# Kernel tuning notes

Measured on AMD Instinct MI355X. Metric: run time of the kernel, lower is better.

The kernel has to match this reference:

```python
import jax, jax.numpy as jnp
import numpy as np

B, N1, N2, E = 8, 32, 32, 256
H = 8                 # num_heads == args.vir_heads
KD = E // H           # key dim per head = 32
HD = E // H           # head dim (value_dim == embed_dim)
L = N1 * N2           # 1024 tokens
SCALING = KD ** -0.5
LN_EPS = 1e-5


def _rel_pos_2d():
    # RetNetRelPosDeform2D with zero offsets (vir_use_deformable=False)
    half = 1.0 / 10000.0 ** jnp.linspace(0.0, 1.0, KD // 2)
    angle = jnp.repeat(half, 2)                                   # (KD,) interleaved pairs
    decay = jnp.log(1.0 - 2.0 ** (-2.0 - 5.0 * jnp.arange(H, dtype=jnp.float32) / H))  # (H,)
    i1 = jnp.arange(N1, dtype=jnp.float32)
    i2 = jnp.arange(N2, dtype=jnp.float32)
    index_k = (i1[:, None] + i2[None, :]).reshape(L)              # (L,)
    sin_k = jnp.sin(index_k[:, None] * angle[None, :])            # (L, KD)
    cos_k = jnp.cos(index_k[:, None] * angle[None, :])
    # zero offsets => index_q == index_k, broadcast over (B, H)
    sin_q = sin_k[None, None]                                     # (1,1,L,KD)
    cos_q = cos_k[None, None]
    # Manhattan distance decay mask on the 2D grid
    d = (jnp.abs(i1[:, None, None, None] - i1[None, None, :, None])
         + jnp.abs(i2[None, :, None, None] - i2[None, None, None, :])).reshape(L, L)
    mask = jnp.exp(d[None, :, :] * decay[:, None, None])          # (H, L, L)
    mask = jnp.nan_to_num(mask)
    mask = mask / jnp.sqrt(mask.sum(-1, keepdims=True))
    return sin_q, cos_q, sin_k, cos_k, mask


def rotate_every_two(x):
    x1 = x[..., ::2]
    x2 = x[..., 1::2]
    return jnp.stack((-x2, x1), axis=-1).reshape(x.shape)


def theta_shift(x, sin, cos):
    return x * cos + rotate_every_two(x) * sin


def setup_inputs() -> dict:
    key = jax.random.key(0)
    ks = jax.random.split(key, 5)
    gain_qkv = 2.0 ** -2.5 * (6.0 / (E + E)) ** 0.5  # xavier_uniform bound scale
    gain_o = 2.0 ** -1 * (6.0 / (E + E)) ** 0.5
    x = jax.random.normal(ks[0], (B, N1, N2, E), dtype=jnp.float32)
    Wq = jax.random.uniform(ks[1], (E, E), jnp.float32, -gain_qkv, gain_qkv)
    Wk = jax.random.uniform(ks[2], (E, E), jnp.float32, -gain_qkv, gain_qkv)
    Wv = jax.random.uniform(ks[3], (E, E), jnp.float32, -gain_qkv, gain_qkv)
    Wo = jax.random.uniform(ks[4], (E, E), jnp.float32, -gain_o, gain_o)
    ln_g = jnp.ones((HD,), jnp.float32)
    ln_b = jnp.zeros((HD,), jnp.float32)
    return {"x": x, "Wq": Wq, "Wk": Wk, "Wv": Wv, "Wo": Wo, "ln_g": ln_g, "ln_b": ln_b}


def reference(x, Wq, Wk, Wv, Wo, ln_g, ln_b):
    sin_q, cos_q, sin_k, cos_k, mask = _rel_pos_2d()
    xf = x.reshape(B, L, E)
    q = (xf @ Wq.T).reshape(B, L, H, KD).transpose(0, 2, 1, 3)    # (B,H,L,KD)
    k = (xf @ Wk.T * SCALING).reshape(B, L, H, KD).transpose(0, 2, 1, 3)
    vr = (xf @ Wv.T).reshape(B, L, H, HD).transpose(0, 2, 1, 3)   # (B,H,L,HD)
    qr = theta_shift(q, sin_q, cos_q)
    kr = theta_shift(k, sin_k[None, None], cos_k[None, None])
    qk = jnp.einsum('bhqd,bhkd->bhqk', qr, kr) * mask[None]       # (B,H,L,L)
    den = jnp.clip(jax.lax.stop_gradient(jnp.abs(qk)).sum(-1, keepdims=True), 1.0, 5e4)
    qk = qk / den
    out = jnp.einsum('bhqk,bhkd->bhqd', qk, vr).transpose(0, 2, 1, 3)  # (B,L,H,HD)
    mu = out.mean(-1, keepdims=True)
    var = out.var(-1, keepdims=True)
    out = (out - mu) / jnp.sqrt(var + LN_EPS) * ln_g + ln_b       # per-head LayerNorm
    out = jax.nn.gelu(out.reshape(B, L, H * HD), approximate=False)
    out = out @ Wo.T
    return out.reshape(B, N1, N2, E)
```

## Files before the change

kernel.cpp:

```cpp
#include <hip/hip_runtime.h>
#include <math.h>

typedef unsigned short u16;
typedef unsigned int u32;
typedef __bf16 bf16x8 __attribute__((ext_vector_type(8)));
typedef float f32x4 __attribute__((ext_vector_type(4)));

#define SCALING 0.17677669529663687f
#define LOG2E 1.44269504088896f
#define LOG2_10000 13.287712379549449f

__device__ __forceinline__ u16 f2bf(float f) {
    u32 u; __builtin_memcpy(&u, &f, 4);
    u = u + 0x7FFFu + ((u >> 16) & 1u);
    return (u16)(u >> 16);
}
__device__ __forceinline__ u32 fbits(float f) {
    u32 u; __builtin_memcpy(&u, &f, 4); return u;
}
__device__ __forceinline__ u32 pack_bf16(float lo, float hi) {
    return __builtin_amdgcn_perm(fbits(hi) + 0x8000u, fbits(lo) + 0x8000u, 0x07060302u);
}
__device__ __forceinline__ f32x4 mfma16(bf16x8 a, bf16x8 b, f32x4 c) {
    return __builtin_amdgcn_mfma_f32_16x16x32_bf16(a, b, c, 0, 0, 0);
}
__device__ __forceinline__ float decay_l2(int h) {
    return logf(1.0f - exp2f(-2.0f - 0.625f * (float)h)) * LOG2E;
}

__global__ __launch_bounds__(256) void cvt_kernel(
    const float* __restrict__ x,
    const float* __restrict__ Wq, const float* __restrict__ Wk,
    const float* __restrict__ Wv, const float* __restrict__ Wo,
    u16* __restrict__ xb, u16* __restrict__ wb) {
    int bid = blockIdx.x;
    const float* src; u16* dst; int off;
    if (bid < 1024) { src = x; dst = xb; off = bid * 2048; }
    else {
        int wsel = (bid - 1024) >> 5;
        src = (wsel == 0) ? Wq : (wsel == 1) ? Wk : (wsel == 2) ? Wv : Wo;
        dst = wb + wsel * 65536;
        off = ((bid - 1024) & 31) * 2048;
    }
    int i = off + threadIdx.x * 8;
    float4 a = *(const float4*)&src[i];
    float4 b = *(const float4*)&src[i + 4];
    union { int4 v; u16 s[8]; } t;
    t.s[0] = f2bf(a.x); t.s[1] = f2bf(a.y); t.s[2] = f2bf(a.z); t.s[3] = f2bf(a.w);
    t.s[4] = f2bf(b.x); t.s[5] = f2bf(b.y); t.s[6] = f2bf(b.z); t.s[7] = f2bf(b.w);
    *(int4*)&dst[i] = t.v;
}

__global__ __launch_bounds__(256) void gemm_bt_kernel(
    const u16* __restrict__ A, const u16* __restrict__ Wb,
    u16* __restrict__ O0, u16* __restrict__ O1, u16* __restrict__ O2,
    float* __restrict__ Of, int mode_base) {
    __shared__ __align__(16) u16 As[64 * 136];
    __shared__ __align__(16) u16 Ws[64 * 136];
    int z = blockIdx.z;
    const u16* W = Wb + z * 65536;
    u16* O = (z == 0) ? O0 : (z == 1) ? O1 : O2;
    int mode = mode_base + z;
    int n0 = blockIdx.x * 64, r0 = blockIdx.y * 64;
    int tid = threadIdx.x;
    int w = tid >> 6, lane = tid & 63, ln = lane & 15, quad = lane >> 4;
    f32x4 acc[4] = {};
#pragma unroll
    for (int ch = 0; ch < 2; ch++) {
        int k0 = ch * 128;
        if (ch) __syncthreads();
#pragma unroll
        for (int i = 0; i < 4; i++) {
            int c = tid + i * 256;
            int row = c >> 4, seg = c & 15;
            *(int4*)&As[row * 136 + seg * 8] = *(const int4*)&A[(long)(r0 + row) * 256 + k0 + seg * 8];
            *(int4*)&Ws[row * 136 + seg * 8] = *(const int4*)&W[(long)(n0 + row) * 256 + k0 + seg * 8];
        }
        __syncthreads();
#pragma unroll
        for (int kt = 0; kt < 4; kt++) {
            bf16x8 a = *(const bf16x8*)&As[(w * 16 + ln) * 136 + kt * 32 + quad * 8];
#pragma unroll
            for (int nt = 0; nt < 4; nt++) {
                bf16x8 b = *(const bf16x8*)&Ws[(nt * 16 + ln) * 136 + kt * 32 + quad * 8];
                acc[nt] = mfma16(a, b, acc[nt]);
            }
        }
    }
    int rowg = r0 + w * 16 + quad * 4;
    if (mode == 3) {
#pragma unroll
        for (int nt = 0; nt < 4; nt++) {
            int e = n0 + nt * 16 + ln;
#pragma unroll
            for (int r = 0; r < 4; r++)
                Of[(long)(rowg + r) * 256 + e] = acc[nt][r];
        }
        return;
    }
    float scl = (mode == 1) ? SCALING : 1.0f;
#pragma unroll
    for (int nt = 0; nt < 4; nt++) {
        int e = n0 + nt * 16 + ln;
        int d = e & 31, hh = e >> 5;
        float ang = exp2f(-LOG2_10000 * (1.0f / 15.0f) * (float)(d >> 1));
#pragma unroll
        for (int r = 0; r < 4; r++) {
            int gi = rowg + r;
            int b = gi >> 10, l = gi & 1023;
            float v = acc[nt][r] * scl;
            float p = __shfl_xor(v, 1);
            float res;
            if (mode == 2) {
                res = v;
            } else {
                float idx = (float)((l >> 5) + (l & 31));
                float sv, cv;
                __sincosf(idx * ang, &sv, &cv);
                res = (d & 1) ? (v * cv + p * sv) : (v * cv - p * sv);
            }
            O[(((long)(b * 8 + hh)) * 1024 + l) * 32 + d] = f2bf(res);
        }
    }
}

__global__ __launch_bounds__(256) void attn_kernel(
    const u16* __restrict__ qr, const u16* __restrict__ kr, const u16* __restrict__ vr,
    const float* __restrict__ lng, const float* __restrict__ lnb,
    u16* __restrict__ out) {
    __shared__ __align__(16) u16 Qs[64 * 40];
    __shared__ __align__(16) u16 Ks[2][64 * 40];
    __shared__ __align__(16) u32 VtW[2][32 * 36];
    __shared__ __align__(16) u32 PsW[4][16 * 36];
    __shared__ float Tt[64];
    __shared__ float Ss[32];
    __shared__ float lngS[32], lnbS[32];
    int b = blockIdx.z, h = blockIdx.y, q0 = blockIdx.x * 64;
    int tid = threadIdx.x, w = tid >> 6, lane = tid & 63, ln = lane & 15, quad = lane >> 4;
    long bh = b * 8 + h;
    const u16* qb = qr + bh * 32768;
    const u16* kb = kr + bh * 32768;
    const u16* vb = vr + bh * 32768;
    float dec = decay_l2(h);
    {
        int row = tid >> 2, seg = tid & 3;
        *(int4*)&Qs[row * 40 + seg * 8] = *(const int4*)&qb[(q0 + row) * 32 + seg * 8];
    }
    if (tid < 63) Tt[tid] = exp2f(dec * (float)tid);
    if (tid >= 64 && tid < 96) { lngS[tid - 64] = lng[tid - 64]; lnbS[tid - 64] = lnb[tid - 64]; }
    int krow = tid >> 2, kseg = tid & 3;
    int vp = tid >> 3, vseg = tid & 7;
    int4 kreg = *(const int4*)&kb[(long)krow * 32 + kseg * 8];
    int2 v0 = *(const int2*)&vb[(long)(vp * 2) * 32 + vseg * 4];
    int2 v1 = *(const int2*)&vb[(long)(vp * 2 + 1) * 32 + vseg * 4];
    __syncthreads();
    if (tid < 32) {
        float s = 0.0f;
#pragma unroll
        for (int b2 = 0; b2 < 32; b2++) s += Tt[abs(tid - b2)];
        Ss[tid] = s;
    }
    *(int4*)&Ks[0][krow * 40 + kseg * 8] = kreg;
    VtW[0][(vseg * 4 + 0) * 36 + vp] = __builtin_amdgcn_perm(v1.x, v0.x, 0x05040100u);
    VtW[0][(vseg * 4 + 1) * 36 + vp] = __builtin_amdgcn_perm(v1.x, v0.x, 0x07060302u);
    VtW[0][(vseg * 4 + 2) * 36 + vp] = __builtin_amdgcn_perm(v1.y, v0.y, 0x05040100u);
    VtW[0][(vseg * 4 + 3) * 36 + vp] = __builtin_amdgcn_perm(v1.y, v0.y, 0x07060302u);
    kreg = *(const int4*)&kb[(long)(64 + krow) * 32 + kseg * 8];
    v0 = *(const int2*)&vb[(long)(64 + vp * 2) * 32 + vseg * 4];
    v1 = *(const int2*)&vb[(long)(64 + vp * 2 + 1) * 32 + vseg * 4];
    __syncthreads();
    int q = q0 + w * 16 + ln;
    int q1i = q >> 5, q2i = q & 31;
    float rqv = rsqrtf(Ss[q1i] * Ss[q2i]);
    bf16x8 aq = *(const bf16x8*)&Qs[(w * 16 + ln) * 40 + quad * 8];
    float bt[2][4];
#pragma unroll
    for (int s2 = 0; s2 < 2; s2++)
#pragma unroll
        for (int r = 0; r < 4; r++)
            bt[s2][r] = Tt[abs(q2i - (s2 * 16 + quad * 4 + r))];
    f32x4 accO0 = {}, accO1 = {};
    float den = 0.0f;
    u32* psw = &PsW[w][0];
    for (int kt = 0; kt < 16; kt++) {
        int cur = kt & 1;
        float a0 = Tt[abs(q1i - 2 * kt)] * rqv;
        float a1 = Tt[abs(q1i - 2 * kt - 1)] * rqv;
        const u16* ksb = &Ks[cur][0];
        const u32* vtb = &VtW[cur][0];
#pragma unroll
        for (int nt = 0; nt < 4; nt++) {
            bf16x8 ak = *(const bf16x8*)&ksb[(nt * 16 + ln) * 40 + quad * 8];
            f32x4 s = mfma16(ak, aq, (f32x4){0.f, 0.f, 0.f, 0.f});
            float aa = (nt & 2) ? a1 : a0;
            float p0 = s[0] * aa * bt[nt & 1][0];
            float p1 = s[1] * aa * bt[nt & 1][1];
            float p2 = s[2] * aa * bt[nt & 1][2];
            float p3 = s[3] * aa * bt[nt & 1][3];
            den += fabsf(p0); den += fabsf(p1); den += fabsf(p2); den += fabsf(p3);
            int2 pw;
            pw.x = (int)pack_bf16(p0, p1);
            pw.y = (int)pack_bf16(p2, p3);
            *(int2*)&psw[ln * 36 + nt * 8 + quad * 2] = pw;
        }
#pragma unroll
        for (int c = 0; c < 2; c++) {
            bf16x8 bp  = *(const bf16x8*)&psw[ln * 36 + c * 16 + quad * 4];
            bf16x8 av0 = *(const bf16x8*)&vtb[(ln)      * 36 + c * 16 + quad * 4];
            bf16x8 av1 = *(const bf16x8*)&vtb[(16 + ln) * 36 + c * 16 + quad * 4];
            accO0 = mfma16(av0, bp, accO0);
            accO1 = mfma16(av1, bp, accO1);
        }
        if (kt < 15) {
            int nb = 1 - cur;
            *(int4*)&Ks[nb][krow * 40 + kseg * 8] = kreg;
            VtW[nb][(vseg * 4 + 0) * 36 + vp] = __builtin_amdgcn_perm(v1.x, v0.x, 0x05040100u);
            VtW[nb][(vseg * 4 + 1) * 36 + vp] = __builtin_amdgcn_perm(v1.x, v0.x, 0x07060302u);
            VtW[nb][(vseg * 4 + 2) * 36 + vp] = __builtin_amdgcn_perm(v1.y, v0.y, 0x05040100u);
            VtW[nb][(vseg * 4 + 3) * 36 + vp] = __builtin_amdgcn_perm(v1.y, v0.y, 0x07060302u);
            if (kt < 14) {
                int t2 = (kt + 2) * 64;
                kreg = *(const int4*)&kb[(long)(t2 + krow) * 32 + kseg * 8];
                v0 = *(const int2*)&vb[(long)(t2 + vp * 2) * 32 + vseg * 4];
                v1 = *(const int2*)&vb[(long)(t2 + vp * 2 + 1) * 32 + vseg * 4];
            }
            __syncthreads();
        }
    }
    den += __shfl_xor(den, 16);
    den += __shfl_xor(den, 32);
    float id = 1.0f / fminf(fmaxf(den, 1.0f), 50000.0f);
    float o[8];
#pragma unroll
    for (int r = 0; r < 4; r++) { o[r] = accO0[r] * id; o[4 + r] = accO1[r] * id; }
    float s1 = 0.0f, s2 = 0.0f;
#pragma unroll
    for (int i = 0; i < 8; i++) { s1 += o[i]; s2 += o[i] * o[i]; }
    s1 += __shfl_xor(s1, 16); s1 += __shfl_xor(s1, 32);
    s2 += __shfl_xor(s2, 16); s2 += __shfl_xor(s2, 32);
    float mean = s1 * (1.0f / 32.0f);
    float var = s2 * (1.0f / 32.0f) - mean * mean;
    float rstd = rsqrtf(var + 1e-5f);
    float xg[8];
#pragma unroll
    for (int nv = 0; nv < 2; nv++)
#pragma unroll
        for (int r = 0; r < 4; r++) {
            int d = nv * 16 + quad * 4 + r;
            float xv = (o[nv * 4 + r] - mean) * rstd * lngS[d] + lnbS[d];
            xg[nv * 4 + r] = 0.5f * xv * (1.0f + erff(xv * 0.70710678118654752f));
        }
    u16* orow = out + ((long)(b * 1024 + q)) * 256 + h * 32;
    int2 st0, st1;
    st0.x = (int)pack_bf16(xg[0], xg[1]); st0.y = (int)pack_bf16(xg[2], xg[3]);
    st1.x = (int)pack_bf16(xg[4], xg[5]); st1.y = (int)pack_bf16(xg[6], xg[7]);
    *(int2*)&orow[quad * 4] = st0;
    *(int2*)&orow[16 + quad * 4] = st1;
}

extern "C" void kernel_launch(void* const* d_in, const int* in_sizes, int n_in,
                              void* d_out, int out_size, void* d_ws, size_t ws_size,
                              hipStream_t stream) {
    const float* x   = (const float*)d_in[0];
    const float* Wq  = (const float*)d_in[1];
    const float* Wk  = (const float*)d_in[2];
    const float* Wv  = (const float*)d_in[3];
    const float* Wo  = (const float*)d_in[4];
    const float* lng = (const float*)d_in[5];
    const float* lnb = (const float*)d_in[6];
    float* outp = (float*)d_out;

    u16* xb   = (u16*)d_ws;
    u16* wb   = xb + 2097152;
    u16* qr   = wb + 262144;
    u16* kr   = qr + 2097152;
    u16* vr   = kr + 2097152;
    u16* attn = vr + 2097152;

    cvt_kernel<<<1152, 256, 0, stream>>>(x, Wq, Wk, Wv, Wo, xb, wb);
    gemm_bt_kernel<<<dim3(4, 128, 3), 256, 0, stream>>>(xb, wb, qr, kr, vr, nullptr, 0);
    attn_kernel<<<dim3(16, 8, 8), 256, 0, stream>>>(qr, kr, vr, lng, lnb, attn);
    gemm_bt_kernel<<<dim3(4, 128, 1), 256, 0, stream>>>(attn, wb + 3 * 65536, nullptr, nullptr, nullptr, outp, 3);
}
```

Baseline: 114.8 us.

## Split attention key tiles across two wave groups and precompute rotary table

After: 134.2 us. +16.9%, slower.

```diff
diff --git a/kernel.cpp b/kernel.cpp
--- a/kernel.cpp
+++ b/kernel.cpp
@@ -32,8 +32,18 @@
     const float* __restrict__ x,
     const float* __restrict__ Wq, const float* __restrict__ Wk,
     const float* __restrict__ Wv, const float* __restrict__ Wo,
-    u16* __restrict__ xb, u16* __restrict__ wb) {
+    u16* __restrict__ xb, u16* __restrict__ wb, float2* __restrict__ tc) {
     int bid = blockIdx.x;
+    if (bid >= 1152) {
+        int idx = (bid - 1152) * 256 + threadIdx.x;
+        int l = idx >> 5, d = idx & 31;
+        float ang = exp2f(-LOG2_10000 * (1.0f / 15.0f) * (float)(d >> 1));
+        float idl = (float)((l >> 5) + (l & 31));
+        float sv, cv;
+        __sincosf(idl * ang, &sv, &cv);
+        tc[idx] = make_float2(cv, (d & 1) ? sv : -sv);
+        return;
+    }
     const float* src; u16* dst; int off;
     if (bid < 1024) { src = x; dst = xb; off = bid * 2048; }
     else {
@@ -53,6 +63,7 @@
 
 __global__ __launch_bounds__(256) void gemm_bt_kernel(
     const u16* __restrict__ A, const u16* __restrict__ Wb,
+    const float2* __restrict__ tc,
     u16* __restrict__ O0, u16* __restrict__ O1, u16* __restrict__ O2,
     float* __restrict__ Of, int mode_base) {
     __shared__ __align__(16) u16 As[64 * 136];
@@ -103,7 +114,6 @@
     for (int nt = 0; nt < 4; nt++) {
         int e = n0 + nt * 16 + ln;
         int d = e & 31, hh = e >> 5;
-        float ang = exp2f(-LOG2_10000 * (1.0f / 15.0f) * (float)(d >> 1));
 #pragma unroll
         for (int r = 0; r < 4; r++) {
             int gi = rowg + r;
@@ -114,45 +124,49 @@
             if (mode == 2) {
                 res = v;
             } else {
-                float idx = (float)((l >> 5) + (l & 31));
-                float sv, cv;
-                __sincosf(idx * ang, &sv, &cv);
-                res = (d & 1) ? (v * cv + p * sv) : (v * cv - p * sv);
+                float2 sc = tc[l * 32 + d];
+                res = v * sc.x + p * sc.y;
             }
             O[(((long)(b * 8 + hh)) * 1024 + l) * 32 + d] = f2bf(res);
         }
     }
 }
 
-__global__ __launch_bounds__(256) void attn_kernel(
+__global__ __launch_bounds__(512) void attn_kernel(
     const u16* __restrict__ qr, const u16* __restrict__ kr, const u16* __restrict__ vr,
     const float* __restrict__ lng, const float* __restrict__ lnb,
     u16* __restrict__ out) {
     __shared__ __align__(16) u16 Qs[64 * 40];
     __shared__ __align__(16) u16 Ks[2][64 * 40];
     __shared__ __align__(16) u32 VtW[2][32 * 36];
-    __shared__ __align__(16) u32 PsW[4][16 * 36];
+    __shared__ __align__(16) u32 PsW[8][16 * 20];
     __shared__ float Tt[64];
     __shared__ float Ss[32];
     __shared__ float lngS[32], lnbS[32];
     int b = blockIdx.z, h = blockIdx.y, q0 = blockIdx.x * 64;
     int tid = threadIdx.x, w = tid >> 6, lane = tid & 63, ln = lane & 15, quad = lane >> 4;
+    int wa = w & 3;
+    int half = w >> 2;
     long bh = b * 8 + h;
     const u16* qb = qr + bh * 32768;
     const u16* kb = kr + bh * 32768;
     const u16* vb = vr + bh * 32768;
     float dec = decay_l2(h);
-    {
+    if (tid < 256) {
         int row = tid >> 2, seg = tid & 3;
         *(int4*)&Qs[row * 40 + seg * 8] = *(const int4*)&qb[(q0 + row) * 32 + seg * 8];
     }
     if (tid < 63) Tt[tid] = exp2f(dec * (float)tid);
     if (tid >= 64 && tid < 96) { lngS[tid - 64] = lng[tid - 64]; lnbS[tid - 64] = lnb[tid - 64]; }
     int krow = tid >> 2, kseg = tid & 3;
-    int vp = tid >> 3, vseg = tid & 7;
-    int4 kreg = *(const int4*)&kb[(long)krow * 32 + kseg * 8];
-    int2 v0 = *(const int2*)&vb[(long)(vp * 2) * 32 + vseg * 4];
-    int2 v1 = *(const int2*)&vb[(long)(vp * 2 + 1) * 32 + vseg * 4];
+    int vt = tid - 256, vp = vt >> 3, vseg = vt & 7;
+    int4 kreg; int2 v0, v1;
+    if (tid < 256) {
+        kreg = *(const int4*)&kb[(long)krow * 32 + kseg * 8];
+    } else {
+        v0 = *(const int2*)&vb[(long)(vp * 2) * 32 + vseg * 4];
+        v1 = *(const int2*)&vb[(long)(vp * 2 + 1) * 32 + vseg * 4];
+    }
     __syncthreads();
     if (tid < 32) {
         float s = 0.0f;
@@ -160,19 +174,22 @@
         for (int b2 = 0; b2 < 32; b2++) s += Tt[abs(tid - b2)];
         Ss[tid] = s;
     }
-    *(int4*)&Ks[0][krow * 40 + kseg * 8] = kreg;
-    VtW[0][(vseg * 4 + 0) * 36 + vp] = __builtin_amdgcn_perm(v1.x, v0.x, 0x05040100u);
-    VtW[0][(vseg * 4 + 1) * 36 + vp] = __builtin_amdgcn_perm(v1.x, v0.x, 0x07060302u);
-    VtW[0][(vseg * 4 + 2) * 36 + vp] = __builtin_amdgcn_perm(v1.y, v0.y, 0x05040100u);
-    VtW[0][(vseg * 4 + 3) * 36 + vp] = __builtin_amdgcn_perm(v1.y, v0.y, 0x07060302u);
-    kreg = *(const int4*)&kb[(long)(64 + krow) * 32 + kseg * 8];
-    v0 = *(const int2*)&vb[(long)(64 + vp * 2) * 32 + vseg * 4];
-    v1 = *(const int2*)&vb[(long)(64 + vp * 2 + 1) * 32 + vseg * 4];
+    if (tid < 256) {
+        *(int4*)&Ks[0][krow * 40 + kseg * 8] = kreg;
+        kreg = *(const int4*)&kb[(long)(64 + krow) * 32 + kseg * 8];
+    } else {
+        VtW[0][(vseg * 4 + 0) * 36 + vp] = __builtin_amdgcn_perm(v1.x, v0.x, 0x05040100u);
+        VtW[0][(vseg * 4 + 1) * 36 + vp] = __builtin_amdgcn_perm(v1.x, v0.x, 0x07060302u);
+        VtW[0][(vseg * 4 + 2) * 36 + vp] = __builtin_amdgcn_perm(v1.y, v0.y, 0x05040100u);
+        VtW[0][(vseg * 4 + 3) * 36 + vp] = __builtin_amdgcn_perm(v1.y, v0.y, 0x07060302u);
+        v0 = *(const int2*)&vb[(long)(64 + vp * 2) * 32 + vseg * 4];
+        v1 = *(const int2*)&vb[(long)(64 + vp * 2 + 1) * 32 + vseg * 4];
+    }
     __syncthreads();
-    int q = q0 + w * 16 + ln;
+    int q = q0 + wa * 16 + ln;
     int q1i = q >> 5, q2i = q & 31;
     float rqv = rsqrtf(Ss[q1i] * Ss[q2i]);
-    bf16x8 aq = *(const bf16x8*)&Qs[(w * 16 + ln) * 40 + quad * 8];
+    bf16x8 aq = *(const bf16x8*)&Qs[(wa * 16 + ln) * 40 + quad * 8];
     float bt[2][4];
 #pragma unroll
     for (int s2 = 0; s2 < 2; s2++)
@@ -184,78 +201,95 @@
     u32* psw = &PsW[w][0];
     for (int kt = 0; kt < 16; kt++) {
         int cur = kt & 1;
-        float a0 = Tt[abs(q1i - 2 * kt)] * rqv;
-        float a1 = Tt[abs(q1i - 2 * kt - 1)] * rqv;
+        float aa = Tt[abs(q1i - 2 * kt - half)] * rqv;
         const u16* ksb = &Ks[cur][0];
         const u32* vtb = &VtW[cur][0];
 #pragma unroll
-        for (int nt = 0; nt < 4; nt++) {
+        for (int j = 0; j < 2; j++) {
+            int nt = 2 * half + j;
             bf16x8 ak = *(const bf16x8*)&ksb[(nt * 16 + ln) * 40 + quad * 8];
             f32x4 s = mfma16(ak, aq, (f32x4){0.f, 0.f, 0.f, 0.f});
-            float aa = (nt & 2) ? a1 : a0;
-            float p0 = s[0] * aa * bt[nt & 1][0];
-            float p1 = s[1] * aa * bt[nt & 1][1];
-            float p2 = s[2] * aa * bt[nt & 1][2];
-            float p3 = s[3] * aa * bt[nt & 1][3];
+            float p0 = s[0] * aa * bt[j][0];
+            float p1 = s[1] * aa * bt[j][1];
+            float p2 = s[2] * aa * bt[j][2];
+            float p3 = s[3] * aa * bt[j][3];
             den += fabsf(p0); den += fabsf(p1); den += fabsf(p2); den += fabsf(p3);
             int2 pw;
             pw.x = (int)pack_bf16(p0, p1);
             pw.y = (int)pack_bf16(p2, p3);
-            *(int2*)&psw[ln * 36 + nt * 8 + quad * 2] = pw;
-        }
-#pragma unroll
-        for (int c = 0; c < 2; c++) {
-            bf16x8 bp  = *(const bf16x8*)&psw[ln * 36 + c * 16 + quad * 4];
-            bf16x8 av0 = *(const bf16x8*)&vtb[(ln)      * 36 + c * 16 + quad * 4];
-            bf16x8 av1 = *(const bf16x8*)&vtb[(16 + ln) * 36 + c * 16 + quad * 4];
+            *(int2*)&psw[ln * 20 + j * 8 + quad * 2] = pw;
+        }
+        {
+            bf16x8 bp  = *(const bf16x8*)&psw[ln * 20 + quad * 4];
+            bf16x8 av0 = *(const bf16x8*)&vtb[(ln)      * 36 + half * 16 + quad * 4];
+            bf16x8 av1 = *(const bf16x8*)&vtb[(16 + ln) * 36 + half * 16 + quad * 4];
             accO0 = mfma16(av0, bp, accO0);
             accO1 = mfma16(av1, bp, accO1);
         }
         if (kt < 15) {
             int nb = 1 - cur;
-            *(int4*)&Ks[nb][krow * 40 + kseg * 8] = kreg;
-            VtW[nb][(vseg * 4 + 0) * 36 + vp] = __builtin_amdgcn_perm(v1.x, v0.x, 0x05040100u);
-            VtW[nb][(vseg * 4 + 1) * 36 + vp] = __builtin_amdgcn_perm(v1.x, v0.x, 0x07060302u);
-            VtW[nb][(vseg * 4 + 2) * 36 + vp] = __builtin_amdgcn_perm(v1.y, v0.y, 0x05040100u);
-            VtW[nb][(vseg * 4 + 3) * 36 + vp] = __builtin_amdgcn_perm(v1.y, v0.y, 0x07060302u);
-            if (kt < 14) {
-                int t2 = (kt + 2) * 64;
-                kreg = *(const int4*)&kb[(long)(t2 + krow) * 32 + kseg * 8];
-                v0 = *(const int2*)&vb[(long)(t2 + vp * 2) * 32 + vseg * 4];
-                v1 = *(const int2*)&vb[(long)(t2 + vp * 2 + 1) * 32 + vseg * 4];
+            if (tid < 256) {
+                *(int4*)&Ks[nb][krow * 40 + kseg * 8] = kreg;
+                if (kt < 14)
+                    kreg = *(const int4*)&kb[(long)((kt + 2) * 64 + krow) * 32 + kseg * 8];
+            } else {
+                VtW[nb][(vseg * 4 + 0) * 36 + vp] = __builtin_amdgcn_perm(v1.x, v0.x, 0x05040100u);
+                VtW[nb][(vseg * 4 + 1) * 36 + vp] = __builtin_amdgcn_perm(v1.x, v0.x, 0x07060302u);
+                VtW[nb][(vseg * 4 + 2) * 36 + vp] = __builtin_amdgcn_perm(v1.y, v0.y, 0x05040100u);
+                VtW[nb][(vseg * 4 + 3) * 36 + vp] = __builtin_amdgcn_perm(v1.y, v0.y, 0x07060302u);
+                if (kt < 14) {
+                    int t2 = (kt + 2) * 64;
+                    v0 = *(const int2*)&vb[(long)(t2 + vp * 2) * 32 + vseg * 4];
+                    v1 = *(const int2*)&vb[(long)(t2 + vp * 2 + 1) * 32 + vseg * 4];
+                }
             }
             __syncthreads();
         }
     }
     den += __shfl_xor(den, 16);
     den += __shfl_xor(den, 32);
-    float id = 1.0f / fminf(fmaxf(den, 1.0f), 50000.0f);
-    float o[8];
-#pragma unroll
-    for (int r = 0; r < 4; r++) { o[r] = accO0[r] * id; o[4 + r] = accO1[r] * id; }
-    float s1 = 0.0f, s2 = 0.0f;
-#pragma unroll
-    for (int i = 0; i < 8; i++) { s1 += o[i]; s2 += o[i] * o[i]; }
-    s1 += __shfl_xor(s1, 16); s1 += __shfl_xor(s1, 32);
-    s2 += __shfl_xor(s2, 16); s2 += __shfl_xor(s2, 32);
-    float mean = s1 * (1.0f / 32.0f);
-    float var = s2 * (1.0f / 32.0f) - mean * mean;
-    float rstd = rsqrtf(var + 1e-5f);
-    float xg[8];
-#pragma unroll
-    for (int nv = 0; nv < 2; nv++)
-#pragma unroll
-        for (int r = 0; r < 4; r++) {
-            int d = nv * 16 + quad * 4 + r;
-            float xv = (o[nv * 4 + r] - mean) * rstd * lngS[d] + lnbS[d];
-            xg[nv * 4 + r] = 0.5f * xv * (1.0f + erff(xv * 0.70710678118654752f));
-        }
-    u16* orow = out + ((long)(b * 1024 + q)) * 256 + h * 32;
-    int2 st0, st1;
-    st0.x = (int)pack_bf16(xg[0], xg[1]); st0.y = (int)pack_bf16(xg[2], xg[3]);
-    st1.x = (int)pack_bf16(xg[4], xg[5]); st1.y = (int)pack_bf16(xg[6], xg[7]);
-    *(int2*)&orow[quad * 4] = st0;
-    *(int2*)&orow[16 + quad * 4] = st1;
+    __syncthreads();
+    float* cmb = (float*)&PsW[0][0];
+    if (half == 1) {
+        float* cp = cmb + (wa * 64 + lane) * 9;
+#pragma unroll
+        for (int r = 0; r < 4; r++) { cp[r] = accO0[r]; cp[4 + r] = accO1[r]; }
+        cp[8] = den;
+    }
+    __syncthreads();
+    if (half == 0) {
+        const float* cp = cmb + (wa * 64 + lane) * 9;
+#pragma unroll
+        for (int r = 0; r < 4; r++) { accO0[r] += cp[r]; accO1[r] += cp[4 + r]; }
+        den += cp[8];
+        float id = 1.0f / fminf(fmaxf(den, 1.0f), 50000.0f);
+        float o[8];
+#pragma unroll
+        for (int r = 0; r < 4; r++) { o[r] = accO0[r] * id; o[4 + r] = accO1[r] * id; }
+        float s1 = 0.0f, s2 = 0.0f;
+#pragma unroll
+        for (int i = 0; i < 8; i++) { s1 += o[i]; s2 += o[i] * o[i]; }
+        s1 += __shfl_xor(s1, 16); s1 += __shfl_xor(s1, 32);
+        s2 += __shfl_xor(s2, 16); s2 += __shfl_xor(s2, 32);
+        float mean = s1 * (1.0f / 32.0f);
+        float var = s2 * (1.0f / 32.0f) - mean * mean;
+        float rstd = rsqrtf(var + 1e-5f);
+        float xg[8];
+#pragma unroll
+        for (int nv = 0; nv < 2; nv++)
+#pragma unroll
+            for (int r = 0; r < 4; r++) {
+                int d = nv * 16 + quad * 4 + r;
+                float xv = (o[nv * 4 + r] - mean) * rstd * lngS[d] + lnbS[d];
+                xg[nv * 4 + r] = 0.5f * xv * (1.0f + erff(xv * 0.70710678118654752f));
+            }
+        u16* orow = out + ((long)(b * 1024 + q)) * 256 + h * 32;
+        int2 st0, st1;
+        st0.x = (int)pack_bf16(xg[0], xg[1]); st0.y = (int)pack_bf16(xg[2], xg[3]);
+        st1.x = (int)pack_bf16(xg[4], xg[5]); st1.y = (int)pack_bf16(xg[6], xg[7]);
+        *(int2*)&orow[quad * 4] = st0;
+        *(int2*)&orow[16 + quad * 4] = st1;
+    }
 }
 
 extern "C" void kernel_launch(void* const* d_in, const int* in_sizes, int n_in,
@@ -276,9 +310,10 @@
     u16* kr   = qr + 2097152;
     u16* vr   = kr + 2097152;
     u16* attn = vr + 2097152;
-
-    cvt_kernel<<<1152, 256, 0, stream>>>(x, Wq, Wk, Wv, Wo, xb, wb);
-    gemm_bt_kernel<<<dim3(4, 128, 3), 256, 0, stream>>>(xb, wb, qr, kr, vr, nullptr, 0);
-    attn_kernel<<<dim3(16, 8, 8), 256, 0, stream>>>(qr, kr, vr, lng, lnb, attn);
-    gemm_bt_kernel<<<dim3(4, 128, 1), 256, 0, stream>>>(attn, wb + 3 * 65536, nullptr, nullptr, nullptr, outp, 3);
-}
+    float2* tc = (float2*)(attn + 2097152);
+
+    cvt_kernel<<<1280, 256, 0, stream>>>(x, Wq, Wk, Wv, Wo, xb, wb, tc);
+    gemm_bt_kernel<<<dim3(4, 128, 3), 256, 0, stream>>>(xb, wb, tc, qr, kr, vr, nullptr, 0);
+    attn_kernel<<<dim3(16, 8, 8), 512, 0, stream>>>(qr, kr, vr, lng, lnb, attn);
+    gemm_bt_kernel<<<dim3(4, 128, 1), 256, 0, stream>>>(attn, wb + 3 * 65536, tc, nullptr, nullptr, nullptr, outp, 3);
+}
```

## Split attention over key halves with combine kernel and precomputed rotary table

Applied to the files above, without the earlier changes.

Result: slower. 121.6 us (+5.9%).

```diff
diff --git a/kernel.cpp b/kernel.cpp
--- a/kernel.cpp
+++ b/kernel.cpp
@@ -32,8 +32,18 @@
     const float* __restrict__ x,
     const float* __restrict__ Wq, const float* __restrict__ Wk,
     const float* __restrict__ Wv, const float* __restrict__ Wo,
-    u16* __restrict__ xb, u16* __restrict__ wb) {
+    u16* __restrict__ xb, u16* __restrict__ wb, float2* __restrict__ tc) {
     int bid = blockIdx.x;
+    if (bid >= 1152) {
+        int idx = (bid - 1152) * 256 + threadIdx.x;
+        int l = idx >> 5, d = idx & 31;
+        float ang = exp2f(-LOG2_10000 * (1.0f / 15.0f) * (float)(d >> 1));
+        float idl = (float)((l >> 5) + (l & 31));
+        float sv, cv;
+        __sincosf(idl * ang, &sv, &cv);
+        tc[idx] = make_float2(cv, (d & 1) ? sv : -sv);
+        return;
+    }
     const float* src; u16* dst; int off;
     if (bid < 1024) { src = x; dst = xb; off = bid * 2048; }
     else {
@@ -53,6 +63,7 @@
 
 __global__ __launch_bounds__(256) void gemm_bt_kernel(
     const u16* __restrict__ A, const u16* __restrict__ Wb,
+    const float2* __restrict__ tc,
     u16* __restrict__ O0, u16* __restrict__ O1, u16* __restrict__ O2,
     float* __restrict__ Of, int mode_base) {
     __shared__ __align__(16) u16 As[64 * 136];
@@ -103,7 +114,6 @@
     for (int nt = 0; nt < 4; nt++) {
         int e = n0 + nt * 16 + ln;
         int d = e & 31, hh = e >> 5;
-        float ang = exp2f(-LOG2_10000 * (1.0f / 15.0f) * (float)(d >> 1));
 #pragma unroll
         for (int r = 0; r < 4; r++) {
             int gi = rowg + r;
@@ -114,80 +124,79 @@
             if (mode == 2) {
                 res = v;
             } else {
-                float idx = (float)((l >> 5) + (l & 31));
-                float sv, cv;
-                __sincosf(idx * ang, &sv, &cv);
-                res = (d & 1) ? (v * cv + p * sv) : (v * cv - p * sv);
+                float2 sc = tc[l * 32 + d];
+                res = v * sc.x + p * sc.y;
             }
             O[(((long)(b * 8 + hh)) * 1024 + l) * 32 + d] = f2bf(res);
         }
     }
 }
 
-__global__ __launch_bounds__(256) void attn_kernel(
+__global__ __launch_bounds__(256) void attn_part_kernel(
     const u16* __restrict__ qr, const u16* __restrict__ kr, const u16* __restrict__ vr,
-    const float* __restrict__ lng, const float* __restrict__ lnb,
-    u16* __restrict__ out) {
-    __shared__ __align__(16) u16 Qs[64 * 40];
-    __shared__ __align__(16) u16 Ks[2][64 * 40];
-    __shared__ __align__(16) u32 VtW[2][32 * 36];
-    __shared__ __align__(16) u32 PsW[4][16 * 36];
-    __shared__ float Tt[64];
-    __shared__ float Ss[32];
-    __shared__ float lngS[32], lnbS[32];
-    int b = blockIdx.z, h = blockIdx.y, q0 = blockIdx.x * 64;
+    float* __restrict__ pO, float* __restrict__ pD) {
+    __shared__ __align__(16) char smem[29056];
+    u16* Qs  = (u16*)smem;
+    u32* PsW = (u32*)smem;
+    u16* Ks0 = (u16*)(smem + 9216);
+    u16* Ks1 = (u16*)(smem + 14336);
+    u32* Vt0 = (u32*)(smem + 19456);
+    u32* Vt1 = (u32*)(smem + 24064);
+    float* Tt = (float*)(smem + 28672);
+    float* Ss = (float*)(smem + 28928);
+    int z = blockIdx.z, b = z >> 1, kh = z & 1, h = blockIdx.y, q0 = blockIdx.x * 64;
     int tid = threadIdx.x, w = tid >> 6, lane = tid & 63, ln = lane & 15, quad = lane >> 4;
     long bh = b * 8 + h;
     const u16* qb = qr + bh * 32768;
-    const u16* kb = kr + bh * 32768;
-    const u16* vb = vr + bh * 32768;
+    const u16* kb = kr + bh * 32768 + kh * 16384;
+    const u16* vb = vr + bh * 32768 + kh * 16384;
     float dec = decay_l2(h);
     {
         int row = tid >> 2, seg = tid & 3;
         *(int4*)&Qs[row * 40 + seg * 8] = *(const int4*)&qb[(q0 + row) * 32 + seg * 8];
     }
     if (tid < 63) Tt[tid] = exp2f(dec * (float)tid);
-    if (tid >= 64 && tid < 96) { lngS[tid - 64] = lng[tid - 64]; lnbS[tid - 64] = lnb[tid - 64]; }
     int krow = tid >> 2, kseg = tid & 3;
     int vp = tid >> 3, vseg = tid & 7;
     int4 kreg = *(const int4*)&kb[(long)krow * 32 + kseg * 8];
     int2 v0 = *(const int2*)&vb[(long)(vp * 2) * 32 + vseg * 4];
     int2 v1 = *(const int2*)&vb[(long)(vp * 2 + 1) * 32 + vseg * 4];
     __syncthreads();
+    bf16x8 aq = *(const bf16x8*)&Qs[(w * 16 + ln) * 40 + quad * 8];
+    int q = q0 + w * 16 + ln;
+    int q1i = q >> 5, q2i = q & 31;
+    float bt[2][4];
+#pragma unroll
+    for (int s2 = 0; s2 < 2; s2++)
+#pragma unroll
+        for (int r = 0; r < 4; r++)
+            bt[s2][r] = Tt[abs(q2i - (s2 * 16 + quad * 4 + r))];
     if (tid < 32) {
         float s = 0.0f;
 #pragma unroll
         for (int b2 = 0; b2 < 32; b2++) s += Tt[abs(tid - b2)];
         Ss[tid] = s;
     }
-    *(int4*)&Ks[0][krow * 40 + kseg * 8] = kreg;
-    VtW[0][(vseg * 4 + 0) * 36 + vp] = __builtin_amdgcn_perm(v1.x, v0.x, 0x05040100u);
-    VtW[0][(vseg * 4 + 1) * 36 + vp] = __builtin_amdgcn_perm(v1.x, v0.x, 0x07060302u);
-    VtW[0][(vseg * 4 + 2) * 36 + vp] = __builtin_amdgcn_perm(v1.y, v0.y, 0x05040100u);
-    VtW[0][(vseg * 4 + 3) * 36 + vp] = __builtin_amdgcn_perm(v1.y, v0.y, 0x07060302u);
+    *(int4*)&Ks0[krow * 40 + kseg * 8] = kreg;
+    Vt0[(vseg * 4 + 0) * 36 + vp] = __builtin_amdgcn_perm(v1.x, v0.x, 0x05040100u);
+    Vt0[(vseg * 4 + 1) * 36 + vp] = __builtin_amdgcn_perm(v1.x, v0.x, 0x07060302u);
+    Vt0[(vseg * 4 + 2) * 36 + vp] = __builtin_amdgcn_perm(v1.y, v0.y, 0x05040100u);
+    Vt0[(vseg * 4 + 3) * 36 + vp] = __builtin_amdgcn_perm(v1.y, v0.y, 0x07060302u);
     kreg = *(const int4*)&kb[(long)(64 + krow) * 32 + kseg * 8];
     v0 = *(const int2*)&vb[(long)(64 + vp * 2) * 32 + vseg * 4];
     v1 = *(const int2*)&vb[(long)(64 + vp * 2 + 1) * 32 + vseg * 4];
     __syncthreads();
-    int q = q0 + w * 16 + ln;
-    int q1i = q >> 5, q2i = q & 31;
     float rqv = rsqrtf(Ss[q1i] * Ss[q2i]);
-    bf16x8 aq = *(const bf16x8*)&Qs[(w * 16 + ln) * 40 + quad * 8];
-    float bt[2][4];
-#pragma unroll
-    for (int s2 = 0; s2 < 2; s2++)
-#pragma unroll
-        for (int r = 0; r < 4; r++)
-            bt[s2][r] = Tt[abs(q2i - (s2 * 16 + quad * 4 + r))];
     f32x4 accO0 = {}, accO1 = {};
     float den = 0.0f;
-    u32* psw = &PsW[w][0];
-    for (int kt = 0; kt < 16; kt++) {
+    u32* psw = &PsW[w * 16 * 36];
+    for (int kt = 0; kt < 8; kt++) {
         int cur = kt & 1;
-        float a0 = Tt[abs(q1i - 2 * kt)] * rqv;
-        float a1 = Tt[abs(q1i - 2 * kt - 1)] * rqv;
-        const u16* ksb = &Ks[cur][0];
-        const u32* vtb = &VtW[cur][0];
+        int ktg = kh * 8 + kt;
+        float a0 = Tt[abs(q1i - 2 * ktg)] * rqv;
+        float a1 = Tt[abs(q1i - 2 * ktg - 1)] * rqv;
+        const u16* ksb = cur ? Ks1 : Ks0;
+        const u32* vtb = cur ? Vt1 : Vt0;
 #pragma unroll
         for (int nt = 0; nt < 4; nt++) {
             bf16x8 ak = *(const bf16x8*)&ksb[(nt * 16 + ln) * 40 + quad * 8];
@@ -211,14 +220,15 @@
             accO0 = mfma16(av0, bp, accO0);
             accO1 = mfma16(av1, bp, accO1);
         }
-        if (kt < 15) {
-            int nb = 1 - cur;
-            *(int4*)&Ks[nb][krow * 40 + kseg * 8] = kreg;
-            VtW[nb][(vseg * 4 + 0) * 36 + vp] = __builtin_amdgcn_perm(v1.x, v0.x, 0x05040100u);
-            VtW[nb][(vseg * 4 + 1) * 36 + vp] = __builtin_amdgcn_perm(v1.x, v0.x, 0x07060302u);
-            VtW[nb][(vseg * 4 + 2) * 36 + vp] = __builtin_amdgcn_perm(v1.y, v0.y, 0x05040100u);
-            VtW[nb][(vseg * 4 + 3) * 36 + vp] = __builtin_amdgcn_perm(v1.y, v0.y, 0x07060302u);
-            if (kt < 14) {
+        if (kt < 7) {
+            u16* ksn = cur ? Ks0 : Ks1;
+            u32* vtn = cur ? Vt0 : Vt1;
+            *(int4*)&ksn[krow * 40 + kseg * 8] = kreg;
+            vtn[(vseg * 4 + 0) * 36 + vp] = __builtin_amdgcn_perm(v1.x, v0.x, 0x05040100u);
+            vtn[(vseg * 4 + 1) * 36 + vp] = __builtin_amdgcn_perm(v1.x, v0.x, 0x07060302u);
+            vtn[(vseg * 4 + 2) * 36 + vp] = __builtin_amdgcn_perm(v1.y, v0.y, 0x05040100u);
+            vtn[(vseg * 4 + 3) * 36 + vp] = __builtin_amdgcn_perm(v1.y, v0.y, 0x07060302u);
+            if (kt < 6) {
                 int t2 = (kt + 2) * 64;
                 kreg = *(const int4*)&kb[(long)(t2 + krow) * 32 + kseg * 8];
                 v0 = *(const int2*)&vb[(long)(t2 + vp * 2) * 32 + vseg * 4];
@@ -229,33 +239,48 @@
     }
     den += __shfl_xor(den, 16);
     den += __shfl_xor(den, 32);
+    long base = ((long)(bh * 2 + kh) * 1024 + q) * 32;
+    *(f32x4*)&pO[base + quad * 4] = accO0;
+    *(f32x4*)&pO[base + 16 + quad * 4] = accO1;
+    if (quad == 0) pD[(bh * 2 + kh) * 1024 + q] = den;
+}
+
+__global__ __launch_bounds__(256) void combine_kernel(
+    const float* __restrict__ pO, const float* __restrict__ pD,
+    const float* __restrict__ lng, const float* __restrict__ lnb,
+    u16* __restrict__ attn) {
+    int tid = threadIdx.x;
+    int row = blockIdx.x * 32 + (tid >> 3);
+    int l8 = tid & 7;
+    int q = row & 1023, bh = row >> 10;
+    long i0 = ((long)(bh * 2) * 1024 + q) * 32 + l8 * 4;
+    f32x4 a = *(const f32x4*)&pO[i0];
+    f32x4 c = *(const f32x4*)&pO[i0 + 32768];
+    float den = pD[(bh * 2) * 1024 + q] + pD[(bh * 2 + 1) * 1024 + q];
     float id = 1.0f / fminf(fmaxf(den, 1.0f), 50000.0f);
-    float o[8];
-#pragma unroll
-    for (int r = 0; r < 4; r++) { o[r] = accO0[r] * id; o[4 + r] = accO1[r] * id; }
-    float s1 = 0.0f, s2 = 0.0f;
-#pragma unroll
-    for (int i = 0; i < 8; i++) { s1 += o[i]; s2 += o[i] * o[i]; }
-    s1 += __shfl_xor(s1, 16); s1 += __shfl_xor(s1, 32);
-    s2 += __shfl_xor(s2, 16); s2 += __shfl_xor(s2, 32);
+    float o[4]; float s1 = 0.0f, s2 = 0.0f;
+#pragma unroll
+    for (int r = 0; r < 4; r++) {
+        o[r] = (a[r] + c[r]) * id;
+        s1 += o[r]; s2 += o[r] * o[r];
+    }
+#pragma unroll
+    for (int m = 1; m < 8; m <<= 1) { s1 += __shfl_xor(s1, m); s2 += __shfl_xor(s2, m); }
     float mean = s1 * (1.0f / 32.0f);
     float var = s2 * (1.0f / 32.0f) - mean * mean;
     float rstd = rsqrtf(var + 1e-5f);
-    float xg[8];
-#pragma unroll
-    for (int nv = 0; nv < 2; nv++)
-#pragma unroll
-        for (int r = 0; r < 4; r++) {
-            int d = nv * 16 + quad * 4 + r;
-            float xv = (o[nv * 4 + r] - mean) * rstd * lngS[d] + lnbS[d];
-            xg[nv * 4 + r] = 0.5f * xv * (1.0f + erff(xv * 0.70710678118654752f));
-        }
-    u16* orow = out + ((long)(b * 1024 + q)) * 256 + h * 32;
-    int2 st0, st1;
-    st0.x = (int)pack_bf16(xg[0], xg[1]); st0.y = (int)pack_bf16(xg[2], xg[3]);
-    st1.x = (int)pack_bf16(xg[4], xg[5]); st1.y = (int)pack_bf16(xg[6], xg[7]);
-    *(int2*)&orow[quad * 4] = st0;
-    *(int2*)&orow[16 + quad * 4] = st1;
+    float xg[4];
+#pragma unroll
+    for (int r = 0; r < 4; r++) {
+        int d = l8 * 4 + r;
+        float xv = (o[r] - mean) * rstd * lng[d] + lnb[d];
+        xg[r] = 0.5f * xv * (1.0f + erff(xv * 0.70710678118654752f));
+    }
+    int b = bh >> 3, h = bh & 7;
+    int2 st;
+    st.x = (int)pack_bf16(xg[0], xg[1]);
+    st.y = (int)pack_bf16(xg[2], xg[3]);
+    *(int2*)&attn[((long)(b * 1024 + q)) * 256 + h * 32 + l8 * 4] = st;
 }
 
 extern "C" void kernel_launch(void* const* d_in, const int* in_sizes, int n_in,
@@ -276,9 +301,13 @@
     u16* kr   = qr + 2097152;
     u16* vr   = kr + 2097152;
     u16* attn = vr + 2097152;
-
-    cvt_kernel<<<1152, 256, 0, stream>>>(x, Wq, Wk, Wv, Wo, xb, wb);
-    gemm_bt_kernel<<<dim3(4, 128, 3), 256, 0, stream>>>(xb, wb, qr, kr, vr, nullptr, 0);
-    attn_kernel<<<dim3(16, 8, 8), 256, 0, stream>>>(qr, kr, vr, lng, lnb, attn);
-    gemm_bt_kernel<<<dim3(4, 128, 1), 256, 0, stream>>>(attn, wb + 3 * 65536, nullptr, nullptr, nullptr, outp, 3);
-}
+    float2* tc = (float2*)(attn + 2097152);
+    float* pO = (float*)(tc + 32768);
+    float* pD = pO + 4194304;
+
+    cvt_kernel<<<1280, 256, 0, stream>>>(x, Wq, Wk, Wv, Wo, xb, wb, tc);
+    gemm_bt_kernel<<<dim3(4, 128, 3), 256, 0, stream>>>(xb, wb, tc, qr, kr, vr, nullptr, 0);
+    attn_part_kernel<<<dim3(16, 8, 16), 256, 0, stream>>>(qr, kr, vr, pO, pD);
+    combine_kernel<<<2048, 256, 0, stream>>>(pO, pD, lng, lnb, attn);
+    gemm_bt_kernel<<<dim3(4, 128, 1), 256, 0, stream>>>(attn, wb + 3 * 65536, tc, nullptr, nullptr, nullptr, outp, 3);
+}
```
